# Optimization experiments

Measured on AMD Instinct MI355X. Metric: run time of the kernel, lower is better.

## Reference

```python
import jax, jax.numpy as jnp
import numpy as np

DEV_VDW, VDW_N, MAXV, MINV, DM_MIN = 0.2, 6.0, 0.0356, 0.0178, 0.5


def setup_inputs() -> dict:
    key = jax.random.key(0)
    ks = iter(jax.random.split(key, 64))
    B, N1, N2, D, L = 8, 128, 256, 128, 3
    f = jnp.float32
    nrm = lambda shape, s=0.05: jax.random.normal(next(ks), shape, f) * s
    ligand_h = jax.random.normal(next(ks), (B, N1, 54), f)
    target_h = jax.random.normal(next(ks), (B, N2, 54), f)
    def adj(n):
        a = (jax.random.uniform(next(ks), (B, n, n)) < 0.08).astype(f)
        a = jnp.maximum(a, jnp.swapaxes(a, 1, 2))
        return jnp.maximum(a, jnp.eye(n, dtype=f))
    ligand_adj = adj(N1)
    target_adj = adj(N2)
    interaction_indice = jax.random.uniform(next(ks), (B, 3, N1, N2), f)
    ligand_pos = jax.random.normal(next(ks), (B, N1, 3), f) * 2.0
    target_pos = jax.random.normal(next(ks), (B, N2, 3), f) * 4.0
    rotor = jax.random.uniform(next(ks), (B,), f) * 10.0
    ligand_vdw_radii = 1.2 + 0.8 * jax.random.uniform(next(ks), (B, N1), f)
    target_vdw_radii = 1.2 + 0.8 * jax.random.uniform(next(ks), (B, N2), f)
    return dict(
        ligand_h=ligand_h, ligand_adj=ligand_adj, target_h=target_h, target_adj=target_adj,
        interaction_indice=interaction_indice, ligand_pos=ligand_pos, target_pos=target_pos,
        rotor=rotor, ligand_vdw_radii=ligand_vdw_radii, target_vdw_radii=target_vdw_radii,
        ligand_valid=jnp.ones((B, N1), f), target_valid=jnp.ones((B, N2), f),
        ligand_non_metal=jnp.ones((B, N1), f), target_non_metal=jnp.ones((B, N2), f),
        emb_w=nrm((54, D)),
        gat_w=nrm((L, D, D)), gat_b=jnp.zeros((L, D), f), gat_att=nrm((L, D, D)),
        gat_gate_w=nrm((L, 2 * D, 1)), gat_gate_b=jnp.zeros((L, 1), f),
        int_wt_w=nrm((L, D, D)), int_wt_b=jnp.zeros((L, D), f),
        int_mt_w=nrm((L, D, D)), int_mt_b=jnp.zeros((L, D), f),
        gru_w_ih=nrm((L, 3 * D, D)), gru_w_hh=nrm((L, 3 * D, D)),
        gru_b_ih=jnp.zeros((L, 3 * D), f), gru_b_hh=jnp.zeros((L, 3 * D), f),
        A_w1=nrm((2 * D, D)), A_b1=jnp.zeros((D,), f), A_w2=nrm((D, 1)), A_b2=jnp.zeros((1,), f),
        B_w1=nrm((2 * D, D)), B_b1=jnp.zeros((D,), f), B_w2=nrm((D, 1)), B_b2=jnp.zeros((1,), f),
        hbond_coeff=jnp.array([1.0], f), hydrophobic_coeff=jnp.array([0.5], f),
        rotor_coeff=jnp.array([0.5], f),
    )


def reference(ligand_h, ligand_adj, target_h, target_adj, interaction_indice, ligand_pos,
              target_pos, rotor, ligand_vdw_radii, target_vdw_radii, ligand_valid,
              target_valid, ligand_non_metal, target_non_metal, emb_w, gat_w, gat_b,
              gat_att, gat_gate_w, gat_gate_b, int_wt_w, int_wt_b, int_mt_w, int_mt_b,
              gru_w_ih, gru_w_hh, gru_b_ih, gru_b_hh, A_w1, A_b1, A_w2, A_b2, B_w1, B_b1,
              B_w2, B_b2, hbond_coeff, hydrophobic_coeff, rotor_coeff):
    B, D, L = ligand_h.shape[0], emb_w.shape[1], gat_w.shape[0]

    def dist(lpos):
        diff = lpos[:, :, None, :] - target_pos[:, None, :, :]
        dm = jnp.sqrt((diff * diff).sum(-1) + 1e-10)
        return jnp.where(dm < DM_MIN, 1e10, dm)

    dm = dist(ligand_pos)

    def gat(x, adj, i):
        nt = x @ gat_w[i] + gat_b[i]                                   # [B,N,D]
        ea = jnp.einsum('bjl,bkl->bjk', nt @ gat_att[i], nt)
        ea = ea + jnp.swapaxes(ea, 1, 2)
        aw = jax.nn.softmax(jnp.where(adj > 1e-6, ea, -9e15), axis=-1) * adj
        out = jax.nn.relu(jnp.einsum('bij,bjd->bid', aw, nt))
        gate = jax.nn.sigmoid(jnp.concatenate([x, out], -1) @ gat_gate_w[i] + gat_gate_b[i])
        return gate * x + (1.0 - gate) * out

    lh = ligand_h @ emb_w
    th = target_h @ emb_w
    for i in range(L):
        lh = gat(lh, ligand_adj, i)
        th = gat(th, target_adj, i)

    adj12 = jax.lax.stop_gradient(dm)
    adj12 = jnp.where(adj12 > 5.0, 0.0, adj12)
    adj12 = jnp.where(adj12 > 1e-3, 1.0, 0.0)
    adj21 = jnp.swapaxes(adj12, 1, 2)

    def inter(a1, a2, ev, i):
        t1 = a1 @ int_wt_w[i] + int_wt_b[i]
        m2 = a2 @ int_mt_w[i] + int_mt_b[i]                            # [B,N2,D]
        t2 = (m2[:, None, :, :] * ev[..., None]).max(axis=2)           # [B,N1,D]
        msg = jax.nn.relu(t1 + t2)
        gi = msg @ gru_w_ih[i].T + gru_b_ih[i]
        gh = a1 @ gru_w_hh[i].T + gru_b_hh[i]
        i_r, i_z, i_n = jnp.split(gi, 3, -1)
        h_r, h_z, h_n = jnp.split(gh, 3, -1)
        r = jax.nn.sigmoid(i_r + h_r)
        z = jax.nn.sigmoid(i_z + h_z)
        n = jnp.tanh(i_n + r * h_n)
        return (1.0 - z) * n + z * a1

    for i in range(L):
        lh, th = inter(lh, th, adj12, i), inter(th, lh, adj21, i)

    N1, N2 = lh.shape[1], th.shape[1]
    h_cat = jnp.concatenate([
        jnp.broadcast_to(lh[:, :, None, :], (B, N1, N2, D)),
        jnp.broadcast_to(th[:, None, :, :], (B, N1, N2, D))], -1)      # [B,N1,N2,2D]

    A_raw = jax.nn.sigmoid(jax.nn.relu(h_cat @ A_w1 + A_b1) @ A_w2 + A_b2)[..., 0]
    B_raw = jnp.tanh(jax.nn.relu(h_cat @ B_w1 + B_b1) @ B_w2 + B_b2)[..., 0] * DEV_VDW
    dm0 = ligand_vdw_radii[:, :, None] + target_vdw_radii[:, None, :] + B_raw
    valid_pair = ligand_non_metal[:, :, None] * target_non_metal[:, None, :]
    A_vdw = A_raw * (MAXV - MINV) + MINV

    def energies_of(dm):
        dm0c = jnp.where(dm0 < 1e-4, 1.0, dm0)
        r6 = (dm0c / dm) ** VDW_N
        evdw = A_vdw * (jnp.minimum(r6 * r6 - 2.0 * r6, 100.0) * valid_pair)
        vdw_val = evdw.sum((1, 2))[:, None]
        dmd = dm - dm0
        def hb(Aind):
            r = jnp.clip(dmd * Aind / -0.7, 0.0, 1.0) * -(hbond_coeff[0] * hbond_coeff[0])
            return r.sum((1, 2))[:, None]
        hbond = hb(interaction_indice[:, 0])
        metal = hb(interaction_indice[:, 1])
        hp = jnp.clip((-dmd + 1.5) * interaction_indice[:, 2], 0.0, 1.0)
        hp = hp * -(hydrophobic_coeff[0] * hydrophobic_coeff[0])
        e = jnp.concatenate([vdw_val, hbond, metal, hp.sum((1, 2))[:, None]], -1)
        return e / (1.0 + rotor_coeff[0] * rotor_coeff[0] * rotor[:, None])

    energies = energies_of(dm)
    esum = lambda p: energies_of(dist(p)).sum()
    g = jax.grad(esum)(ligand_pos)
    der1 = (g.sum(1) ** 2).mean()
    der2 = -jax.grad(lambda p: jax.grad(esum)(p).sum())(ligand_pos).sum((1, 2)).mean()
    return energies, der1, der2
```

## Files before the change

kernel.cpp:

```cpp
#include <hip/hip_runtime.h>
#include <math.h>

#define BB 8
#define N1C 128
#define N2C 256
#define DC 128
#define NHC 54
#define ROWS_L 1024
#define ROWS_T 2048
#define ROWS_ALL 3072

__device__ __forceinline__ float wredSum(float v) {
#pragma unroll
  for (int o = 32; o > 0; o >>= 1) v += __shfl_down(v, o);
  return v;
}
__device__ float blockSum(float v) {
  __shared__ float red[9];
  v = wredSum(v);
  int lane = threadIdx.x & 63, wid = threadIdx.x >> 6;
  __syncthreads();
  if (lane == 0) red[wid] = v;
  __syncthreads();
  if (threadIdx.x == 0) {
    float s = 0.f;
    int nw = (blockDim.x + 63) >> 6;
    for (int i = 0; i < nw; ++i) s += red[i];
    red[8] = s;
  }
  __syncthreads();
  return red[8];
}

__global__ __launch_bounds__(256) void k_prep(
    const float* __restrict__ LP, const float* __restrict__ TP,
    float* __restrict__ AD, const float* __restrict__ LH,
    const float* __restrict__ TH, const float* __restrict__ EW,
    float* __restrict__ H0, const float* __restrict__ GWp,
    const float* __restrict__ GBp, const float* __restrict__ ATT,
    float* __restrict__ WA, float* __restrict__ bA,
    const float* __restrict__ IH, const float* __restrict__ HH,
    float* __restrict__ GIHT, float* __restrict__ GHHT) {
  int bid = blockIdx.x, tid = threadIdx.x;
  if (bid < 1024) {
    long idx = (long)bid * 256 + tid;
    int j = idx & (N2C - 1);
    long t = idx >> 8;
    int i = (int)(t & (N1C - 1));
    int b = (int)(t >> 7);
    float dx = LP[((long)b * N1C + i) * 3 + 0] - TP[((long)b * N2C + j) * 3 + 0];
    float dy = LP[((long)b * N1C + i) * 3 + 1] - TP[((long)b * N2C + j) * 3 + 1];
    float dz = LP[((long)b * N1C + i) * 3 + 2] - TP[((long)b * N2C + j) * 3 + 2];
    float d = sqrtf(dx * dx + dy * dy + dz * dz + 1e-10f);
    if (d < 0.5f) d = 1e10f;
    AD[idx] = (d <= 5.0f && d > 1e-3f) ? 1.f : 0.f;
  } else if (bid < 1024 + 384) {
    int r0 = (bid - 1024) * 8;
    __shared__ float xs[8][NHC];
    for (int t = tid; t < 8 * NHC; t += 256) {
      int rr = r0 + t / NHC, c = t % NHC;
      xs[t / NHC][c] = (rr < ROWS_L) ? LH[(long)rr * NHC + c]
                                     : TH[(long)(rr - ROWS_L) * NHC + c];
    }
    __syncthreads();
    int d = tid & 127, rb = (tid >> 7) * 4;
    float a[4] = {0.f, 0.f, 0.f, 0.f};
#pragma unroll 6
    for (int k = 0; k < NHC; ++k) {
      float wv = EW[(long)k * DC + d];
#pragma unroll
      for (int r = 0; r < 4; ++r) a[r] += xs[rb + r][k] * wv;
    }
#pragma unroll
    for (int r = 0; r < 4; ++r) H0[(long)(r0 + rb + r) * DC + d] = a[r];
  } else if (bid < 1024 + 384 + 99) {
    int q = bid - 1408;
    int l = q / 33, bx = q % 33;
    const float* Wl = GWp + (long)l * DC * DC;
    const float* Al = ATT + (long)l * DC * DC;
    if (bx == 32) {
      if (tid < 128) {
        float acc = 0.f;
#pragma unroll 8
        for (int m = 0; m < DC; ++m)
          acc += GBp[l * DC + m] * Al[(long)m * DC + tid];
        bA[l * DC + tid] = acc;
      }
    } else {
      __shared__ float xs2[4][DC];
      int r0 = bx * 4;
      for (int t = tid; t < 4 * DC; t += 256)
        xs2[t >> 7][t & 127] = Wl[(long)r0 * DC + t];
      __syncthreads();
      if (tid < 128) {
        int d = tid;
        float a0 = 0.f, a1 = 0.f, a2 = 0.f, a3 = 0.f;
#pragma unroll 8
        for (int m = 0; m < DC; ++m) {
          float av = Al[(long)m * DC + d];
          a0 += xs2[0][m] * av;
          a1 += xs2[1][m] * av;
          a2 += xs2[2][m] * av;
          a3 += xs2[3][m] * av;
        }
        float* out = WA + (long)l * DC * DC + (long)r0 * DC + d;
        out[0] = a0;
        out[DC] = a1;
        out[2 * DC] = a2;
        out[3 * DC] = a3;
      }
    }
  } else {
    long idx = (long)(bid - 1507) * 256 + tid;
    if (idx < 6L * 49152) {
      int a = (int)(idx / 49152);
      int rem = (int)(idx % 49152);
      int l = a >> 1, whh = a & 1;
      int c = rem / 384, rr = rem % 384;
      const float* src = (whh ? HH : IH) + (long)l * 49152;
      float* dst = (whh ? GHHT : GIHT) + (long)l * 49152;
      dst[(long)c * 384 + rr] = src[(long)rr * 128 + c];
    }
  }
}

__global__ __launch_bounds__(256) void k_lin2h(
    const float* __restrict__ X, const float* __restrict__ W1,
    const float* __restrict__ b1, const float* __restrict__ W2,
    const float* __restrict__ b2, float* __restrict__ Y1, float* __restrict__ Y2,
    int rpb, int trans) {
  int r0 = blockIdx.x * 8;
  __shared__ float xs_t[DC][8];
  int tid = threadIdx.x;
  for (int t = tid; t < 8 * DC; t += 256) {
    int r = t >> 7, c = t & 127;
    xs_t[c][r] = X[(long)(r0 + r) * DC + c];
  }
  __syncthreads();
  int h = tid >> 7, d = tid & 127;
  const float* W = h ? W2 : W1;
  const float* bp = h ? b2 : b1;
  float* Y = h ? Y2 : Y1;
  float a0 = 0.f, a1 = 0.f, a2 = 0.f, a3 = 0.f;
  float a4 = 0.f, a5 = 0.f, a6 = 0.f, a7 = 0.f;
#pragma unroll 8
  for (int k = 0; k < DC; ++k) {
    float4 x0 = *(const float4*)&xs_t[k][0];
    float4 x1 = *(const float4*)&xs_t[k][4];
    float wv = W[(long)k * DC + d];
    a0 = fmaf(x0.x, wv, a0);
    a1 = fmaf(x0.y, wv, a1);
    a2 = fmaf(x0.z, wv, a2);
    a3 = fmaf(x0.w, wv, a3);
    a4 = fmaf(x1.x, wv, a4);
    a5 = fmaf(x1.y, wv, a5);
    a6 = fmaf(x1.z, wv, a6);
    a7 = fmaf(x1.w, wv, a7);
  }
  float bv = bp ? bp[d] : 0.f;
  float v[8] = {a0 + bv, a1 + bv, a2 + bv, a3 + bv,
                a4 + bv, a5 + bv, a6 + bv, a7 + bv};
  if (!trans) {
#pragma unroll
    for (int r = 0; r < 8; ++r) Y[(long)(r0 + r) * DC + d] = v[r];
  } else {
    int b = r0 / rpb, rin = r0 - b * rpb;
#pragma unroll
    for (int r = 0; r < 8; ++r)
      Y[((long)b * DC + d) * rpb + rin + r] = v[r];
  }
}

__global__ __launch_bounds__(256) void k_ea2(const float* __restrict__ NTp,
                                             const float* __restrict__ E1p,
                                             const float* __restrict__ ADJL,
                                             const float* __restrict__ ADJT,
                                             float* __restrict__ EAL,
                                             float* __restrict__ EAT) {
  int id = blockIdx.x;
  int N, base, j0, k0, b;
  const float* ADJ;
  float* EA;
  if (id < 64) {
    b = id >> 3;
    int rem = id & 7;
    N = N1C;
    base = b * N1C;
    j0 = (rem >> 1) * 32;
    k0 = (rem & 1) * 64;
    ADJ = ADJL + (long)b * N1C * N1C;
    EA = EAL + (long)b * N1C * N1C;
  } else {
    int q = id - 64;
    b = q >> 5;
    int rem = q & 31;
    N = N2C;
    base = ROWS_L + b * N2C;
    j0 = (rem >> 2) * 32;
    k0 = (rem & 3) * 64;
    ADJ = ADJT + (long)b * N2C * N2C;
    EA = EAT + (long)b * N2C * N2C;
  }
  __shared__ float aj_e1[32][34], aj_nt[32][34];
  __shared__ float bk_e1[32][68], bk_nt[32][68];
  int tid = threadIdx.x, tx = tid & 15, ty = tid >> 4;
  float acc[2][4];
#pragma unroll
  for (int r = 0; r < 2; ++r)
#pragma unroll
    for (int c = 0; c < 4; ++c) acc[r][c] = 0.f;
  for (int kc = 0; kc < DC; kc += 32) {
    __syncthreads();
    for (int t = tid; t < 1024; t += 256) {
      int kk = t & 31, rr = t >> 5;
      aj_e1[kk][rr] = E1p[(long)(base + j0 + rr) * DC + kc + kk];
      aj_nt[kk][rr] = NTp[(long)(base + j0 + rr) * DC + kc + kk];
    }
    for (int t = tid; t < 2048; t += 256) {
      int kk = t & 31, cc = t >> 5;
      bk_e1[kk][cc] = E1p[(long)(base + k0 + cc) * DC + kc + kk];
      bk_nt[kk][cc] = NTp[(long)(base + k0 + cc) * DC + kc + kk];
    }
    __syncthreads();
#pragma unroll
    for (int kk = 0; kk < 32; ++kk) {
      float2 ae = *(const float2*)&aj_e1[kk][ty * 2];
      float2 an = *(const float2*)&aj_nt[kk][ty * 2];
      float4 bn = *(const float4*)&bk_nt[kk][tx * 4];
      float4 be = *(const float4*)&bk_e1[kk][tx * 4];
      acc[0][0] = fmaf(ae.x, bn.x, fmaf(an.x, be.x, acc[0][0]));
      acc[0][1] = fmaf(ae.x, bn.y, fmaf(an.x, be.y, acc[0][1]));
      acc[0][2] = fmaf(ae.x, bn.z, fmaf(an.x, be.z, acc[0][2]));
      acc[0][3] = fmaf(ae.x, bn.w, fmaf(an.x, be.w, acc[0][3]));
      acc[1][0] = fmaf(ae.y, bn.x, fmaf(an.y, be.x, acc[1][0]));
      acc[1][1] = fmaf(ae.y, bn.y, fmaf(an.y, be.y, acc[1][1]));
      acc[1][2] = fmaf(ae.y, bn.z, fmaf(an.y, be.z, acc[1][2]));
      acc[1][3] = fmaf(ae.y, bn.w, fmaf(an.y, be.w, acc[1][3]));
    }
  }
#pragma unroll
  for (int r = 0; r < 2; ++r) {
    long rowi = (long)(j0 + ty * 2 + r) * N + k0 + tx * 4;
    float4 ad = *(const float4*)&ADJ[rowi];
    float4 o;
    o.x = (ad.x > 1e-6f) ? acc[r][0] : -9e15f;
    o.y = (ad.y > 1e-6f) ? acc[r][1] : -9e15f;
    o.z = (ad.z > 1e-6f) ? acc[r][2] : -9e15f;
    o.w = (ad.w > 1e-6f) ? acc[r][3] : -9e15f;
    *(float4*)&EA[rowi] = o;
  }
}

__global__ __launch_bounds__(512) void k_smagg3(
    const float* __restrict__ EAL, const float* __restrict__ EAT,
    const float* __restrict__ NTp, const float* __restrict__ Xp,
    const float* __restrict__ GW, const float* __restrict__ GB,
    float* __restrict__ Y) {
  int z = blockIdx.z;
  int N = z ? N2C : N1C;
  if (blockIdx.x * 16 >= N) return;
  int ls = z ? 8 : 7;
  int baseRow = z ? ROWS_L : 0;
  const float* EA = z ? EAT : EAL;
  int b = blockIdx.y, i0 = blockIdx.x * 16;
  __shared__ float ps[16][N2C + 4];
  __shared__ float col[32][DC + 4];
  __shared__ float red[16];
  int tid = threadIdx.x;
  const float* EAb = EA + (long)b * N * N + (long)i0 * N;
  for (int t = tid; t < 16 * N; t += 512)
    ps[t >> ls][t & (N - 1)] = EAb[t];
  __syncthreads();
  int r = tid >> 5, l = tid & 31;
  {
    float m = -INFINITY;
    for (int k = l; k < N; k += 32) m = fmaxf(m, ps[r][k]);
#pragma unroll
    for (int o = 16; o > 0; o >>= 1) m = fmaxf(m, __shfl_xor(m, o));
    float s = 0.f;
    for (int k = l; k < N; k += 32) {
      float p = expf(ps[r][k] - m);
      ps[r][k] = p;
      s += p;
    }
#pragma unroll
    for (int o = 16; o > 0; o >>= 1) s += __shfl_xor(s, o);
    float inv = 1.f / s;
    for (int k = l; k < N; k += 32) ps[r][k] *= inv;
  }
  int d0 = l * 4;
  float a0 = 0.f, a1 = 0.f, a2 = 0.f, a3 = 0.f;
  const float* NTb = NTp + (long)(baseRow + b * N) * DC;
  for (int k0 = 0; k0 < N; k0 += 32) {
    __syncthreads();
    for (int t = tid; t < 32 * DC; t += 512)
      col[t >> 7][t & 127] = NTb[(long)(k0 + (t >> 7)) * DC + (t & 127)];
    __syncthreads();
#pragma unroll 8
    for (int kk = 0; kk < 32; ++kk) {
      float4 c4 = *(const float4*)&col[kk][d0];
      float p = ps[r][k0 + kk];
      a0 = fmaf(p, c4.x, a0);
      a1 = fmaf(p, c4.y, a1);
      a2 = fmaf(p, c4.z, a2);
      a3 = fmaf(p, c4.w, a3);
    }
  }
  float4 gwd = *(const float4*)&GW[d0];
  float4 gwo = *(const float4*)&GW[DC + d0];
  float4 x4 = *(const float4*)&Xp[(long)(baseRow + b * N + i0 + r) * DC + d0];
  float o0 = fmaxf(a0, 0.f), o1 = fmaxf(a1, 0.f);
  float o2 = fmaxf(a2, 0.f), o3 = fmaxf(a3, 0.f);
  float part = x4.x * gwd.x + o0 * gwo.x + x4.y * gwd.y + o1 * gwo.y +
               x4.z * gwd.z + o2 * gwo.z + x4.w * gwd.w + o3 * gwo.w;
#pragma unroll
  for (int o = 16; o > 0; o >>= 1) part += __shfl_xor(part, o);
  if (l == 0) red[r] = part;
  __syncthreads();
  float g = 1.f / (1.f + expf(-(red[r] + GB[0])));
  float4 y;
  y.x = g * x4.x + (1.f - g) * o0;
  y.y = g * x4.y + (1.f - g) * o1;
  y.z = g * x4.z + (1.f - g) * o2;
  y.w = g * x4.w + (1.f - g) * o3;
  *(float4*)&Y[(long)(baseRow + b * N + i0 + r) * DC + d0] = y;
}

__global__ __launch_bounds__(256) void k_msg2v(const float* __restrict__ T1,
                                               const float* __restrict__ M2,
                                               const float* __restrict__ EV,
                                               float* __restrict__ MSG) {
  int z = blockIdx.z, b = blockIdx.y;
  int Ni = z ? N2C : N1C, Nj = z ? N1C : N2C;
  if (blockIdx.x * 8 >= Ni) return;
  int t1off = z ? ROWS_L : 0, m2off = z ? 0 : ROWS_L;
  long ev_is = z ? 1L : (long)N2C, ev_js = z ? (long)N2C : 1L;
  int i0 = blockIdx.x * 8;
  __shared__ float m2s[32][DC + 4];
  __shared__ float evs[8][36];
  int dgrp = threadIdx.x & 31, row = threadIdx.x >> 5;
  int d0 = dgrp * 4;
  float a0 = -INFINITY, a1 = -INFINITY, a2 = -INFINITY, a3 = -INFINITY;
  const float* M2b = M2 + (long)(m2off + b * Nj) * DC;
  const float* EVb = EV + (long)b * (N1C * N2C);
  for (int j0 = 0; j0 < Nj; j0 += 32) {
    __syncthreads();
    for (int t = threadIdx.x; t < 32 * DC; t += 256)
      m2s[t >> 7][t & 127] = M2b[(long)(j0 + (t >> 7)) * DC + (t & 127)];
    for (int t = threadIdx.x; t < 256; t += 256)
      evs[t >> 5][t & 31] =
          EVb[(long)(i0 + (t >> 5)) * ev_is + (long)(j0 + (t & 31)) * ev_js];
    __syncthreads();
#pragma unroll 8
    for (int jj = 0; jj < 32; ++jj) {
      float4 m4 = *(const float4*)&m2s[jj][d0];
      float e = evs[row][jj];
      a0 = fmaxf(a0, m4.x * e);
      a1 = fmaxf(a1, m4.y * e);
      a2 = fmaxf(a2, m4.z * e);
      a3 = fmaxf(a3, m4.w * e);
    }
  }
  long grow = t1off + (long)b * Ni + i0 + row;
  float4 t4 = *(const float4*)&T1[grow * DC + d0];
  float4 o;
  o.x = fmaxf(t4.x + a0, 0.f);
  o.y = fmaxf(t4.y + a1, 0.f);
  o.z = fmaxf(t4.z + a2, 0.f);
  o.w = fmaxf(t4.w + a3, 0.f);
  *(float4*)&MSG[grow * DC + d0] = o;
}

__global__ __launch_bounds__(384) void k_gruf(
    const float* __restrict__ MSGp, const float* __restrict__ Hp,
    const float* __restrict__ WihT, const float* __restrict__ WhhT,
    const float* __restrict__ bih, const float* __restrict__ bhh,
    float* __restrict__ Y) {
  const int D = DC;
  int r0 = blockIdx.x * 4;
  __shared__ float xs_t[DC][4], hs_t[DC][4];
  __shared__ float gis[4][384], ghs[4][384];
  int tid = threadIdx.x;
  for (int t = tid; t < 4 * DC; t += 384) {
    int r = t >> 7, c = t & 127;
    xs_t[c][r] = MSGp[(long)(r0 + r) * D + c];
    hs_t[c][r] = Hp[(long)(r0 + r) * D + c];
  }
  __syncthreads();
  int dd = tid;
  float ai[4] = {0.f, 0.f, 0.f, 0.f}, ah[4] = {0.f, 0.f, 0.f, 0.f};
#pragma unroll 8
  for (int k = 0; k < DC; ++k) {
    float4 xv = *reinterpret_cast<const float4*>(&xs_t[k][0]);
    float4 hv = *reinterpret_cast<const float4*>(&hs_t[k][0]);
    float wi = WihT[(long)k * 384 + dd];
    float wh = WhhT[(long)k * 384 + dd];
    ai[0] = fmaf(xv.x, wi, ai[0]);
    ai[1] = fmaf(xv.y, wi, ai[1]);
    ai[2] = fmaf(xv.z, wi, ai[2]);
    ai[3] = fmaf(xv.w, wi, ai[3]);
    ah[0] = fmaf(hv.x, wh, ah[0]);
    ah[1] = fmaf(hv.y, wh, ah[1]);
    ah[2] = fmaf(hv.z, wh, ah[2]);
    ah[3] = fmaf(hv.w, wh, ah[3]);
  }
  float bi = bih[dd], bh = bhh[dd];
#pragma unroll
  for (int r = 0; r < 4; ++r) {
    gis[r][dd] = ai[r] + bi;
    ghs[r][dd] = ah[r] + bh;
  }
  __syncthreads();
  for (int t = tid; t < 4 * DC; t += 384) {
    int r = t >> 7, d = t & 127;
    float ir = gis[r][d], iz = gis[r][d + 128], inn = gis[r][d + 256];
    float hr = ghs[r][d], hz = ghs[r][d + 128], hn = ghs[r][d + 256];
    float rg = 1.f / (1.f + expf(-(ir + hr)));
    float zg = 1.f / (1.f + expf(-(iz + hz)));
    float ng = tanhf(inn + rg * hn);
    Y[(long)(r0 + r) * D + d] = (1.f - zg) * ng + zg * hs_t[d][r];
  }
}

__global__ __launch_bounds__(256) void k_pair(
    const float* __restrict__ UA, const float* __restrict__ VAT,
    const float* __restrict__ UB, const float* __restrict__ VBT,
    const float* __restrict__ AW2, const float* __restrict__ AB2,
    const float* __restrict__ BW2, const float* __restrict__ BB2,
    const float* __restrict__ LP, const float* __restrict__ TP,
    const float* __restrict__ LVDW, const float* __restrict__ TVDW,
    const float* __restrict__ LNM, const float* __restrict__ TNM,
    const float* __restrict__ II, const float* __restrict__ HBC,
    const float* __restrict__ HPC, float* __restrict__ PART) {
  const int D = DC, N1 = N1C, N2 = N2C;
  int i0 = blockIdx.x * 2, b = blockIdx.y, j = threadIdx.x;
  __shared__ float ua[2][128], ub[2][128], wa2[128], wb2[128];
  if (j < 128) {
    long rb = ((long)b * N1 + i0) * D + j;
    ua[0][j] = UA[rb];
    ub[0][j] = UB[rb];
    wa2[j] = AW2[j];
    wb2[j] = BW2[j];
  } else {
    int jj = j - 128;
    long rb = ((long)b * N1 + i0 + 1) * D + jj;
    ua[1][jj] = UA[rb];
    ub[1][jj] = UB[rb];
  }
  __syncthreads();
  const float* vat = VAT + (long)b * D * N2;
  const float* vbt = VBT + (long)b * D * N2;
  float dotA[2] = {0.f, 0.f}, dotB[2] = {0.f, 0.f};
#pragma unroll 4
  for (int d = 0; d < D; ++d) {
    float va = vat[(long)d * N2 + j];
    float vb = vbt[(long)d * N2 + j];
    dotA[0] += fmaxf(ua[0][d] + va, 0.f) * wa2[d];
    dotA[1] += fmaxf(ua[1][d] + va, 0.f) * wa2[d];
    dotB[0] += fmaxf(ub[0][d] + vb, 0.f) * wb2[d];
    dotB[1] += fmaxf(ub[1][d] + vb, 0.f) * wb2[d];
  }
  float hb2 = HBC[0] * HBC[0], hp2 = HPC[0] * HPC[0];
  float tx = TP[((long)b * N2 + j) * 3 + 0];
  float ty = TP[((long)b * N2 + j) * 3 + 1];
  float tz = TP[((long)b * N2 + j) * 3 + 2];
  float tvd = TVDW[b * N2 + j];
  float tnm = TNM[b * N2 + j];
  float res[2][8];
#pragma unroll
  for (int ii = 0; ii < 2; ++ii) {
    int i = i0 + ii;
    float A_raw = 1.f / (1.f + expf(-(dotA[ii] + AB2[0])));
    float A_vdw = A_raw * (0.0356f - 0.0178f) + 0.0178f;
    float B_raw = tanhf(dotB[ii] + BB2[0]) * 0.2f;

    float lx = LP[((long)b * N1 + i) * 3 + 0];
    float ly = LP[((long)b * N1 + i) * 3 + 1];
    float lz = LP[((long)b * N1 + i) * 3 + 2];
    float dx = lx - tx, dy = ly - ty, dz = lz - tz;
    float s2 = dx * dx + dy * dy + dz * dz + 1e-10f;
    float draw = sqrtf(s2);
    bool clamped = draw < 0.5f;
    float dmv = clamped ? 1e10f : draw;

    float dm0 = LVDW[b * N1 + i] + tvd + B_raw;
    float dm0c = (dm0 < 1e-4f) ? 1.f : dm0;
    float valid = LNM[b * N1 + i] * tnm;

    float rr = dm0c / dmv;
    float r2 = rr * rr, r6 = r2 * r2 * r2;
    float fv = r6 * r6 - 2.f * r6;
    float evdw = A_vdw * (fminf(fv, 100.f) * valid);

    float dmd = dmv - dm0;
    long ii0x = ((long)b * 3) * N1 * N2 + (long)i * N2 + j;
    float I0 = II[ii0x];
    float I1 = II[ii0x + (long)N1 * N2];
    float I2 = II[ii0x + 2L * N1 * N2];
    float u0 = dmd * I0 / (-0.7f);
    float u1 = dmd * I1 / (-0.7f);
    float vv = (1.5f - dmd) * I2;
    float ehb = fminf(fmaxf(u0, 0.f), 1.f) * (-hb2);
    float emt = fminf(fmaxf(u1, 0.f), 1.f) * (-hb2);
    float ehp = fminf(fmaxf(vv, 0.f), 1.f) * (-hp2);

    float gx = 0.f, gy = 0.f, gz = 0.f, d2t = 0.f;
    if (!clamped) {
      float Ep = 0.f, Epp = 0.f;
      if (fv < 100.f) {
        float c = A_vdw * valid;
        Ep += c * (-12.f) * r6 * (r6 - 1.f) / draw;
        Epp += c * r6 * (156.f * r6 - 84.f) / s2;
      }
      if (u0 > 0.f && u0 < 1.f) Ep += hb2 * I0 * (1.f / 0.7f);
      if (u1 > 0.f && u1 < 1.f) Ep += hb2 * I1 * (1.f / 0.7f);
      if (vv > 0.f && vv < 1.f) Ep += hp2 * I2;
      float invd = 1.f / draw;
      gx = Ep * dx * invd;
      gy = Ep * dy * invd;
      gz = Ep * dz * invd;
      float T = dx + dy + dz;
      float tt = T * T / s2;
      d2t = Epp * tt + Ep * (3.f - tt) * invd;
    }
    res[ii][0] = evdw;
    res[ii][1] = ehb;
    res[ii][2] = emt;
    res[ii][3] = ehp;
    res[ii][4] = gx;
    res[ii][5] = gy;
    res[ii][6] = gz;
    res[ii][7] = d2t;
  }
#pragma unroll
  for (int ii = 0; ii < 2; ++ii) {
    float o[8];
#pragma unroll
    for (int q = 0; q < 8; ++q) o[q] = blockSum(res[ii][q]);
    if (j == 0) {
      float* p = PART + ((long)b * N1 + i0 + ii) * 8;
#pragma unroll
      for (int q = 0; q < 8; ++q) p[q] = o[q];
    }
  }
}

__global__ void k_final(const float* __restrict__ PART, const float* __restrict__ ROT,
                        const float* __restrict__ RC, float* __restrict__ OUT) {
  const int N1 = N1C;
  __shared__ float s[8][8];
  int t = threadIdx.x;
  if (t < 64) {
    int b = t >> 3, k1 = t & 7;
    float acc = 0.f;
    for (int i = 0; i < N1; ++i) acc += PART[((long)b * N1 + i) * 8 + k1];
    s[b][k1] = acc;
  }
  __syncthreads();
  if (t == 0) {
    float rcc = RC[0] * RC[0];
    float der1 = 0.f, der2 = 0.f;
    for (int b = 0; b < 8; ++b) {
      float w = 1.f / (1.f + rcc * ROT[b]);
      OUT[b * 4 + 0] = s[b][0] * w;
      OUT[b * 4 + 1] = s[b][1] * w;
      OUT[b * 4 + 2] = s[b][2] * w;
      OUT[b * 4 + 3] = s[b][3] * w;
      for (int c = 0; c < 3; ++c) {
        float S = s[b][4 + c] * w;
        der1 += S * S;
      }
      der2 += s[b][7] * w;
    }
    OUT[32] = der1 / 24.f;
    OUT[33] = -der2 / 8.f;
  }
}

extern "C" void kernel_launch(void* const* d_in, const int* in_sizes, int n_in,
                              void* d_out, int out_size, void* d_ws, size_t ws_size,
                              hipStream_t stream) {
  (void)in_sizes; (void)n_in; (void)out_size; (void)ws_size;
  const int D = DC;

  const float* ligand_h   = (const float*)d_in[0];
  const float* ligand_adj = (const float*)d_in[1];
  const float* target_h   = (const float*)d_in[2];
  const float* target_adj = (const float*)d_in[3];
  const float* inter_ind  = (const float*)d_in[4];
  const float* ligand_pos = (const float*)d_in[5];
  const float* target_pos = (const float*)d_in[6];
  const float* rotor      = (const float*)d_in[7];
  const float* lvdw       = (const float*)d_in[8];
  const float* tvdw       = (const float*)d_in[9];
  const float* lnm        = (const float*)d_in[12];
  const float* tnm        = (const float*)d_in[13];
  const float* emb_w      = (const float*)d_in[14];
  const float* gat_w      = (const float*)d_in[15];
  const float* gat_b      = (const float*)d_in[16];
  const float* gat_att    = (const float*)d_in[17];
  const float* gat_gate_w = (const float*)d_in[18];
  const float* gat_gate_b = (const float*)d_in[19];
  const float* int_wt_w   = (const float*)d_in[20];
  const float* int_wt_b   = (const float*)d_in[21];
  const float* int_mt_w   = (const float*)d_in[22];
  const float* int_mt_b   = (const float*)d_in[23];
  const float* gru_w_ih   = (const float*)d_in[24];
  const float* gru_w_hh   = (const float*)d_in[25];
  const float* gru_b_ih   = (const float*)d_in[26];
  const float* gru_b_hh   = (const float*)d_in[27];
  const float* A_w1       = (const float*)d_in[28];
  const float* A_b1       = (const float*)d_in[29];
  const float* A_w2       = (const float*)d_in[30];
  const float* A_b2       = (const float*)d_in[31];
  const float* B_w1       = (const float*)d_in[32];
  const float* B_b1       = (const float*)d_in[33];
  const float* B_w2       = (const float*)d_in[34];
  const float* B_b2       = (const float*)d_in[35];
  const float* hb_c       = (const float*)d_in[36];
  const float* hp_c       = (const float*)d_in[37];
  const float* rc_c       = (const float*)d_in[38];

  float* w = (float*)d_ws;
  auto take = [&](size_t n) { float* p = w; w += n; return p; };
  float* H0    = take((size_t)ROWS_ALL * DC);
  float* H1    = take((size_t)ROWS_ALL * DC);
  float* NT    = take((size_t)ROWS_ALL * DC);
  float* E1    = take((size_t)ROWS_ALL * DC);
  float* EAL   = take((size_t)BB * N1C * N1C);
  float* EAT   = take((size_t)BB * N2C * N2C);
  float* ADJ12 = take((size_t)BB * N1C * N2C);
  float* WA    = take((size_t)3 * DC * DC);
  float* bA    = take((size_t)3 * DC);
  float* GIHT  = take((size_t)3 * DC * 384);
  float* GHHT  = take((size_t)3 * DC * 384);
  float* PART  = take((size_t)BB * N1C * 8);
  float* T1  = NT;
  float* M2  = E1;
  float* MSG = EAT;
  float* UA  = EAL;
  float* UB  = EAT;
  float* VAT = NT;
  float* VBT = E1;

  k_prep<<<2659, 256, 0, stream>>>(ligand_pos, target_pos, ADJ12, ligand_h,
                                   target_h, emb_w, H0, gat_w, gat_b, gat_att,
                                   WA, bA, gru_w_ih, gru_w_hh, GIHT, GHHT);

  float *cur = H0, *alt = H1;

  for (int l = 0; l < 3; ++l) {
    k_lin2h<<<ROWS_ALL / 8, 256, 0, stream>>>(
        cur, gat_w + (size_t)l * D * D, gat_b + l * D, WA + (size_t)l * D * D,
        bA + l * D, NT, E1, 1, 0);
    k_ea2<<<320, 256, 0, stream>>>(NT, E1, ligand_adj, target_adj, EAL, EAT);
    k_smagg3<<<dim3(N2C / 16, BB, 2), 512, 0, stream>>>(
        EAL, EAT, NT, cur, gat_gate_w + l * 2 * D, gat_gate_b + l, alt);
    float* t = cur; cur = alt; alt = t;
  }

  for (int l = 0; l < 3; ++l) {
    k_lin2h<<<ROWS_ALL / 8, 256, 0, stream>>>(
        cur, int_wt_w + (size_t)l * D * D, int_wt_b + l * D,
        int_mt_w + (size_t)l * D * D, int_mt_b + l * D, T1, M2, 1, 0);
    k_msg2v<<<dim3(32, 8, 2), 256, 0, stream>>>(T1, M2, ADJ12, MSG);
    k_gruf<<<ROWS_ALL / 4, 384, 0, stream>>>(MSG, cur, GIHT + (size_t)l * D * 384,
                                             GHHT + (size_t)l * D * 384,
                                             gru_b_ih + l * 384,
                                             gru_b_hh + l * 384, alt);
    float* t = cur; cur = alt; alt = t;
  }

  k_lin2h<<<ROWS_L / 8, 256, 0, stream>>>(cur, A_w1, A_b1, B_w1, B_b1, UA, UB,
                                          1, 0);
  k_lin2h<<<ROWS_T / 8, 256, 0, stream>>>(cur + (size_t)ROWS_L * DC,
                                          A_w1 + D * D, nullptr, B_w1 + D * D,
                                          nullptr, VAT, VBT, N2C, 1);

  k_pair<<<dim3(N1C / 2, BB), 256, 0, stream>>>(UA, VAT, UB, VBT, A_w2, A_b2,
                                                B_w2, B_b2, ligand_pos,
                                                target_pos, lvdw, tvdw, lnm,
                                                tnm, inter_ind, hb_c, hp_c,
                                                PART);

  k_final<<<1, 256, 0, stream>>>(PART, rotor, rc_c, (float*)d_out);
}
```

Baseline: 371.4 us.

## Fuse message max-aggregation into GRU kernel and merge final feature projections

```diff
diff --git a/kernel.cpp b/kernel.cpp
--- a/kernel.cpp
+++ b/kernel.cpp
@@ -127,12 +127,12 @@
 __global__ __launch_bounds__(256) void k_lin2h(
     const float* __restrict__ X, const float* __restrict__ W1,
     const float* __restrict__ b1, const float* __restrict__ W2,
-    const float* __restrict__ b2, float* __restrict__ Y1, float* __restrict__ Y2,
-    int rpb, int trans) {
-  int r0 = blockIdx.x * 8;
-  __shared__ float xs_t[DC][8];
+    const float* __restrict__ b2, float* __restrict__ Y1,
+    float* __restrict__ Y2) {
+  int r0 = blockIdx.x * 4;
+  __shared__ float xs_t[DC][4];
   int tid = threadIdx.x;
-  for (int t = tid; t < 8 * DC; t += 256) {
+  for (int t = tid; t < 4 * DC; t += 256) {
     int r = t >> 7, c = t & 127;
     xs_t[c][r] = X[(long)(r0 + r) * DC + c];
   }
@@ -142,32 +142,66 @@
   const float* bp = h ? b2 : b1;
   float* Y = h ? Y2 : Y1;
   float a0 = 0.f, a1 = 0.f, a2 = 0.f, a3 = 0.f;
-  float a4 = 0.f, a5 = 0.f, a6 = 0.f, a7 = 0.f;
 #pragma unroll 8
   for (int k = 0; k < DC; ++k) {
-    float4 x0 = *(const float4*)&xs_t[k][0];
-    float4 x1 = *(const float4*)&xs_t[k][4];
+    float4 xv = *(const float4*)&xs_t[k][0];
     float wv = W[(long)k * DC + d];
-    a0 = fmaf(x0.x, wv, a0);
-    a1 = fmaf(x0.y, wv, a1);
-    a2 = fmaf(x0.z, wv, a2);
-    a3 = fmaf(x0.w, wv, a3);
-    a4 = fmaf(x1.x, wv, a4);
-    a5 = fmaf(x1.y, wv, a5);
-    a6 = fmaf(x1.z, wv, a6);
-    a7 = fmaf(x1.w, wv, a7);
+    a0 = fmaf(xv.x, wv, a0);
+    a1 = fmaf(xv.y, wv, a1);
+    a2 = fmaf(xv.z, wv, a2);
+    a3 = fmaf(xv.w, wv, a3);
   }
   float bv = bp ? bp[d] : 0.f;
-  float v[8] = {a0 + bv, a1 + bv, a2 + bv, a3 + bv,
-                a4 + bv, a5 + bv, a6 + bv, a7 + bv};
-  if (!trans) {
-#pragma unroll
-    for (int r = 0; r < 8; ++r) Y[(long)(r0 + r) * DC + d] = v[r];
+  Y[(long)(r0 + 0) * DC + d] = a0 + bv;
+  Y[(long)(r0 + 1) * DC + d] = a1 + bv;
+  Y[(long)(r0 + 2) * DC + d] = a2 + bv;
+  Y[(long)(r0 + 3) * DC + d] = a3 + bv;
+}
+
+__global__ __launch_bounds__(256) void k_featall(
+    const float* __restrict__ X, const float* __restrict__ Aw1,
+    const float* __restrict__ Ab1, const float* __restrict__ Bw1,
+    const float* __restrict__ Bb1, float* __restrict__ UA,
+    float* __restrict__ UB, float* __restrict__ VAT,
+    float* __restrict__ VBT) {
+  int bid = blockIdx.x;
+  bool lig = bid < 256;
+  int r0 = lig ? bid * 4 : ROWS_L + (bid - 256) * 4;
+  __shared__ float xs_t[DC][4];
+  int tid = threadIdx.x;
+  for (int t = tid; t < 4 * DC; t += 256) {
+    int r = t >> 7, c = t & 127;
+    xs_t[c][r] = X[(long)(r0 + r) * DC + c];
+  }
+  __syncthreads();
+  int h = tid >> 7, d = tid & 127;
+  const float* W = (h ? Bw1 : Aw1) + (lig ? 0 : DC * DC);
+  float a0 = 0.f, a1 = 0.f, a2 = 0.f, a3 = 0.f;
+#pragma unroll 8
+  for (int k = 0; k < DC; ++k) {
+    float4 xv = *(const float4*)&xs_t[k][0];
+    float wv = W[(long)k * DC + d];
+    a0 = fmaf(xv.x, wv, a0);
+    a1 = fmaf(xv.y, wv, a1);
+    a2 = fmaf(xv.z, wv, a2);
+    a3 = fmaf(xv.w, wv, a3);
+  }
+  if (lig) {
+    float bv = h ? Bb1[d] : Ab1[d];
+    float* Y = h ? UB : UA;
+    Y[(long)(r0 + 0) * DC + d] = a0 + bv;
+    Y[(long)(r0 + 1) * DC + d] = a1 + bv;
+    Y[(long)(r0 + 2) * DC + d] = a2 + bv;
+    Y[(long)(r0 + 3) * DC + d] = a3 + bv;
   } else {
-    int b = r0 / rpb, rin = r0 - b * rpb;
-#pragma unroll
-    for (int r = 0; r < 8; ++r)
-      Y[((long)b * DC + d) * rpb + rin + r] = v[r];
+    float* V = h ? VBT : VAT;
+    int q = bid - 256;
+    int b = q >> 6, rin = (q * 4) & 255;
+    float* dst = &V[((long)b * DC + d) * N2C + rin];
+    dst[0] = a0;
+    dst[1] = a1;
+    dst[2] = a2;
+    dst[3] = a3;
   }
 }
 
@@ -326,99 +360,89 @@
   *(float4*)&Y[(long)(baseRow + b * N + i0 + r) * DC + d0] = y;
 }
 
-__global__ __launch_bounds__(256) void k_msg2v(const float* __restrict__ T1,
-                                               const float* __restrict__ M2,
-                                               const float* __restrict__ EV,
-                                               float* __restrict__ MSG) {
-  int z = blockIdx.z, b = blockIdx.y;
-  int Ni = z ? N2C : N1C, Nj = z ? N1C : N2C;
-  if (blockIdx.x * 8 >= Ni) return;
-  int t1off = z ? ROWS_L : 0, m2off = z ? 0 : ROWS_L;
-  long ev_is = z ? 1L : (long)N2C, ev_js = z ? (long)N2C : 1L;
-  int i0 = blockIdx.x * 8;
-  __shared__ float m2s[32][DC + 4];
-  __shared__ float evs[8][36];
-  int dgrp = threadIdx.x & 31, row = threadIdx.x >> 5;
-  int d0 = dgrp * 4;
-  float a0 = -INFINITY, a1 = -INFINITY, a2 = -INFINITY, a3 = -INFINITY;
-  const float* M2b = M2 + (long)(m2off + b * Nj) * DC;
-  const float* EVb = EV + (long)b * (N1C * N2C);
-  for (int j0 = 0; j0 < Nj; j0 += 32) {
-    __syncthreads();
-    for (int t = threadIdx.x; t < 32 * DC; t += 256)
-      m2s[t >> 7][t & 127] = M2b[(long)(j0 + (t >> 7)) * DC + (t & 127)];
-    for (int t = threadIdx.x; t < 256; t += 256)
-      evs[t >> 5][t & 31] =
-          EVb[(long)(i0 + (t >> 5)) * ev_is + (long)(j0 + (t & 31)) * ev_js];
-    __syncthreads();
-#pragma unroll 8
-    for (int jj = 0; jj < 32; ++jj) {
-      float4 m4 = *(const float4*)&m2s[jj][d0];
-      float e = evs[row][jj];
-      a0 = fmaxf(a0, m4.x * e);
-      a1 = fmaxf(a1, m4.y * e);
-      a2 = fmaxf(a2, m4.z * e);
-      a3 = fmaxf(a3, m4.w * e);
-    }
-  }
-  long grow = t1off + (long)b * Ni + i0 + row;
-  float4 t4 = *(const float4*)&T1[grow * DC + d0];
-  float4 o;
-  o.x = fmaxf(t4.x + a0, 0.f);
-  o.y = fmaxf(t4.y + a1, 0.f);
-  o.z = fmaxf(t4.z + a2, 0.f);
-  o.w = fmaxf(t4.w + a3, 0.f);
-  *(float4*)&MSG[grow * DC + d0] = o;
-}
-
-__global__ __launch_bounds__(384) void k_gruf(
-    const float* __restrict__ MSGp, const float* __restrict__ Hp,
+__global__ __launch_bounds__(512) void k_msggru(
+    const float* __restrict__ T1, const float* __restrict__ M2,
+    const float* __restrict__ EV, const float* __restrict__ Hp,
     const float* __restrict__ WihT, const float* __restrict__ WhhT,
     const float* __restrict__ bih, const float* __restrict__ bhh,
     float* __restrict__ Y) {
-  const int D = DC;
   int r0 = blockIdx.x * 4;
+  __shared__ float m2s[32][DC + 4];
+  __shared__ float evs[4][36];
   __shared__ float xs_t[DC][4], hs_t[DC][4];
   __shared__ float gis[4][384], ghs[4][384];
   int tid = threadIdx.x;
-  for (int t = tid; t < 4 * DC; t += 384) {
-    int r = t >> 7, c = t & 127;
-    xs_t[c][r] = MSGp[(long)(r0 + r) * D + c];
-    hs_t[c][r] = Hp[(long)(r0 + r) * D + c];
-  }
-  __syncthreads();
-  int dd = tid;
-  float ai[4] = {0.f, 0.f, 0.f, 0.f}, ah[4] = {0.f, 0.f, 0.f, 0.f};
+  int Nj, m2base, b, i0in;
+  long ev_is, ev_js;
+  if (r0 < ROWS_L) {
+    b = r0 >> 7;
+    i0in = r0 & 127;
+    Nj = N2C;
+    m2base = ROWS_L + b * N2C;
+    ev_is = N2C;
+    ev_js = 1;
+  } else {
+    int q = r0 - ROWS_L;
+    b = q >> 8;
+    i0in = q & 255;
+    Nj = N1C;
+    m2base = b * N1C;
+    ev_is = 1;
+    ev_js = N2C;
+  }
+  const float* EVb = EV + (long)b * (N1C * N2C);
+  int r = tid >> 7, d = tid & 127;
+  float acc = -INFINITY;
+  for (int j0 = 0; j0 < Nj; j0 += 32) {
+    __syncthreads();
+    for (int t = tid; t < 32 * DC; t += 512)
+      m2s[t >> 7][t & 127] = M2[(long)(m2base + j0 + (t >> 7)) * DC + (t & 127)];
+    if (tid < 128)
+      evs[tid >> 5][tid & 31] =
+          EVb[(long)(i0in + (tid >> 5)) * ev_is + (long)(j0 + (tid & 31)) * ev_js];
+    __syncthreads();
 #pragma unroll 8
-  for (int k = 0; k < DC; ++k) {
-    float4 xv = *reinterpret_cast<const float4*>(&xs_t[k][0]);
-    float4 hv = *reinterpret_cast<const float4*>(&hs_t[k][0]);
-    float wi = WihT[(long)k * 384 + dd];
-    float wh = WhhT[(long)k * 384 + dd];
-    ai[0] = fmaf(xv.x, wi, ai[0]);
-    ai[1] = fmaf(xv.y, wi, ai[1]);
-    ai[2] = fmaf(xv.z, wi, ai[2]);
-    ai[3] = fmaf(xv.w, wi, ai[3]);
-    ah[0] = fmaf(hv.x, wh, ah[0]);
-    ah[1] = fmaf(hv.y, wh, ah[1]);
-    ah[2] = fmaf(hv.z, wh, ah[2]);
-    ah[3] = fmaf(hv.w, wh, ah[3]);
-  }
-  float bi = bih[dd], bh = bhh[dd];
-#pragma unroll
-  for (int r = 0; r < 4; ++r) {
-    gis[r][dd] = ai[r] + bi;
-    ghs[r][dd] = ah[r] + bh;
-  }
-  __syncthreads();
-  for (int t = tid; t < 4 * DC; t += 384) {
-    int r = t >> 7, d = t & 127;
-    float ir = gis[r][d], iz = gis[r][d + 128], inn = gis[r][d + 256];
-    float hr = ghs[r][d], hz = ghs[r][d + 128], hn = ghs[r][d + 256];
+    for (int jj = 0; jj < 32; ++jj)
+      acc = fmaxf(acc, m2s[jj][d] * evs[r][jj]);
+  }
+  xs_t[d][r] = fmaxf(T1[(long)(r0 + r) * DC + d] + acc, 0.f);
+  for (int t = tid; t < 4 * DC; t += 512)
+    hs_t[t & 127][t >> 7] = Hp[(long)(r0 + (t >> 7)) * DC + (t & 127)];
+  __syncthreads();
+  if (tid < 384) {
+    int dd = tid;
+    float ai[4] = {0.f, 0.f, 0.f, 0.f}, ah[4] = {0.f, 0.f, 0.f, 0.f};
+#pragma unroll 8
+    for (int k = 0; k < DC; ++k) {
+      float4 xv = *(const float4*)&xs_t[k][0];
+      float4 hv = *(const float4*)&hs_t[k][0];
+      float wi = WihT[(long)k * 384 + dd];
+      float wh = WhhT[(long)k * 384 + dd];
+      ai[0] = fmaf(xv.x, wi, ai[0]);
+      ai[1] = fmaf(xv.y, wi, ai[1]);
+      ai[2] = fmaf(xv.z, wi, ai[2]);
+      ai[3] = fmaf(xv.w, wi, ai[3]);
+      ah[0] = fmaf(hv.x, wh, ah[0]);
+      ah[1] = fmaf(hv.y, wh, ah[1]);
+      ah[2] = fmaf(hv.z, wh, ah[2]);
+      ah[3] = fmaf(hv.w, wh, ah[3]);
+    }
+    float bi = bih[dd], bh = bhh[dd];
+#pragma unroll
+    for (int rr = 0; rr < 4; ++rr) {
+      gis[rr][dd] = ai[rr] + bi;
+      ghs[rr][dd] = ah[rr] + bh;
+    }
+  }
+  __syncthreads();
+  for (int t = tid; t < 4 * DC; t += 512) {
+    int rr = t >> 7, dq = t & 127;
+    float ir = gis[rr][dq], iz = gis[rr][dq + 128], inn = gis[rr][dq + 256];
+    float hr = ghs[rr][dq], hz = ghs[rr][dq + 128], hn = ghs[rr][dq + 256];
     float rg = 1.f / (1.f + expf(-(ir + hr)));
     float zg = 1.f / (1.f + expf(-(iz + hz)));
     float ng = tanhf(inn + rg * hn);
-    Y[(long)(r0 + r) * D + d] = (1.f - zg) * ng + zg * hs_t[d][r];
+    Y[(long)(r0 + rr) * DC + dq] = (1.f - zg) * ng + zg * hs_t[dq][rr];
   }
 }
 
@@ -637,7 +661,6 @@
   float* PART  = take((size_t)BB * N1C * 8);
   float* T1  = NT;
   float* M2  = E1;
-  float* MSG = EAT;
   float* UA  = EAL;
   float* UB  = EAT;
   float* VAT = NT;
@@ -650,9 +673,9 @@
   float *cur = H0, *alt = H1;
 
   for (int l = 0; l < 3; ++l) {
-    k_lin2h<<<ROWS_ALL / 8, 256, 0, stream>>>(
+    k_lin2h<<<ROWS_ALL / 4, 256, 0, stream>>>(
         cur, gat_w + (size_t)l * D * D, gat_b + l * D, WA + (size_t)l * D * D,
-        bA + l * D, NT, E1, 1, 0);
+        bA + l * D, NT, E1);
     k_ea2<<<320, 256, 0, stream>>>(NT, E1, ligand_adj, target_adj, EAL, EAT);
     k_smagg3<<<dim3(N2C / 16, BB, 2), 512, 0, stream>>>(
         EAL, EAT, NT, cur, gat_gate_w + l * 2 * D, gat_gate_b + l, alt);
@@ -660,22 +683,18 @@
   }
 
   for (int l = 0; l < 3; ++l) {
-    k_lin2h<<<ROWS_ALL / 8, 256, 0, stream>>>(
+    k_lin2h<<<ROWS_ALL / 4, 256, 0, stream>>>(
         cur, int_wt_w + (size_t)l * D * D, int_wt_b + l * D,
-        int_mt_w + (size_t)l * D * D, int_mt_b + l * D, T1, M2, 1, 0);
-    k_msg2v<<<dim3(32, 8, 2), 256, 0, stream>>>(T1, M2, ADJ12, MSG);
-    k_gruf<<<ROWS_ALL / 4, 384, 0, stream>>>(MSG, cur, GIHT + (size_t)l * D * 384,
-                                             GHHT + (size_t)l * D * 384,
-                                             gru_b_ih + l * 384,
-                                             gru_b_hh + l * 384, alt);
+        int_mt_w + (size_t)l * D * D, int_mt_b + l * D, T1, M2);
+    k_msggru<<<ROWS_ALL / 4, 512, 0, stream>>>(
+        T1, M2, ADJ12, cur, GIHT + (size_t)l * D * 384,
+        GHHT + (size_t)l * D * 384, gru_b_ih + l * 384, gru_b_hh + l * 384,
+        alt);
     float* t = cur; cur = alt; alt = t;
   }
 
-  k_lin2h<<<ROWS_L / 8, 256, 0, stream>>>(cur, A_w1, A_b1, B_w1, B_b1, UA, UB,
-                                          1, 0);
-  k_lin2h<<<ROWS_T / 8, 256, 0, stream>>>(cur + (size_t)ROWS_L * DC,
-                                          A_w1 + D * D, nullptr, B_w1 + D * D,
-                                          nullptr, VAT, VBT, N2C, 1);
+  k_featall<<<768, 256, 0, stream>>>(cur, A_w1, A_b1, B_w1, B_b1, UA, UB, VAT,
+                                     VBT);
 
   k_pair<<<dim3(N1C / 2, BB), 256, 0, stream>>>(UA, VAT, UB, VBT, A_w2, A_b2,
                                                 B_w2, B_b2, ligand_pos,
```

After: 331.0 us. -10.9%, faster.
